# Optimization experiments

Measured on AMD Instinct MI355X. Metric: run time of the kernel, lower is better.

Reference implementation:

```python
import jax, jax.numpy as jnp
import numpy as np

N_NODES = 50000


def gcn_layer(x, W, b, src, dst, num_nodes):
    """PyG-style GCNConv: add self-loops, symmetric normalization, linear, scatter-add, bias."""
    # linear transform first (PyG applies lin before propagate)
    h = x @ W  # [N, out]
    # add self loops
    loop = jnp.arange(num_nodes, dtype=src.dtype)
    s = jnp.concatenate([src, loop])  # [E+N]
    d = jnp.concatenate([dst, loop])  # [E+N]
    # degree of target nodes (with self loops)
    deg = jax.ops.segment_sum(jnp.ones_like(d, dtype=h.dtype), d, num_segments=num_nodes)
    dis = jnp.where(deg > 0, jax.lax.rsqrt(deg), 0.0)  # deg^{-1/2}
    norm = dis[s] * dis[d]  # [E+N]
    msg = h[s] * norm[:, None]  # gather + scale: [E+N, out]
    out = jax.ops.segment_sum(msg, d, num_segments=num_nodes)  # scatter-add
    return out + b


def setup_inputs() -> dict:
    key = jax.random.key(0)
    ks = jax.random.split(key, 8)
    n, e = N_NODES, 800000
    in_c, hid_c, out_c = 64, 128, 64
    x = jax.random.normal(ks[0], (n, in_c), dtype=jnp.float32)
    edge_index = jax.random.randint(ks[1], (2, e), 0, n, dtype=jnp.int64)
    def glorot(k, fan_in, fan_out):
        lim = np.sqrt(6.0 / (fan_in + fan_out)).astype(np.float32)
        return jax.random.uniform(k, (fan_in, fan_out), jnp.float32, -lim, lim)
    return {
        "x": x,
        "edge_index": edge_index,
        "W1": glorot(ks[2], in_c, hid_c), "b1": jnp.zeros((hid_c,), jnp.float32),
        "W2": glorot(ks[3], hid_c, hid_c), "b2": jnp.zeros((hid_c,), jnp.float32),
        "W3": glorot(ks[4], hid_c, out_c), "b3": jnp.zeros((out_c,), jnp.float32),
    }


def reference(x, edge_index, W1, b1, W2, b2, W3, b3):
    src, dst = edge_index[0], edge_index[1]
    n = x.shape[0]
    h = gcn_layer(x, W1, b1, src, dst, n)
    h = jax.nn.relu(h)
    h = gcn_layer(h, W2, b2, src, dst, n)
    h = jax.nn.relu(h)
    return gcn_layer(h, W3, b3, src, dst, n)
```

## Files before the change

kernel.cpp:

```cpp
#include <hip/hip_runtime.h>
#include <hip/hip_fp16.h>


typedef _Float16 h8 __attribute__((ext_vector_type(8)));
typedef float f32x4 __attribute__((ext_vector_type(4)));

struct alignas(8) Half4 { __half2 lo, hi; };

__device__ inline float4 h4_to_f4(Half4 h) {
    float2 a = __half22float2(h.lo), b = __half22float2(h.hi);
    return make_float4(a.x, a.y, b.x, b.y);
}
__device__ inline Half4 f4_to_h4(float4 v) {
    Half4 h; h.lo = __floats2half2_rn(v.x, v.y); h.hi = __floats2half2_rn(v.z, v.w); return h;
}

#define MAXNB 512


__global__ __launch_bounds__(256) void bucket_count(const int* __restrict__ dst,
                                                    int* __restrict__ bcnt, int e, int nb) {
    __shared__ int h[MAXNB];
    int tid = threadIdx.x;
    for (int i = tid; i < nb; i += 256) h[i] = 0;
    __syncthreads();
    for (int i = blockIdx.x * 256 + tid; i < e; i += gridDim.x * 256)
        atomicAdd(&h[dst[i] >> 7], 1);
    __syncthreads();
    for (int i = tid; i < nb; i += 256) {
        int c = h[i];
        if (c) atomicAdd(&bcnt[i], c);
    }
}


__global__ void scan_buckets(const int* __restrict__ bcnt, int* __restrict__ bbase,
                             int* __restrict__ bcursor, int nb) {
    int lane = threadIdx.x;
    int running = 0;
    for (int base = 0; base < nb; base += 64) {
        int idx = base + lane;
        int v = (idx < nb) ? bcnt[idx] : 0;
        int x = v;
        #pragma unroll
        for (int d = 1; d < 64; d <<= 1) {
            int t = __shfl_up(x, d, 64);
            if (lane >= d) x += t;
        }
        if (idx < nb) { bbase[idx] = running + x - v; bcursor[idx] = running + x - v; }
        running += __shfl(x, 63, 64);
    }
    if (lane == 0) bbase[nb] = running;
}


#define R3_CHUNK 4096

template<bool PACKED>
__global__ __launch_bounds__(256) void bin_edges(const int* __restrict__ src,
                                                 const int* __restrict__ dst,
                                                 int* __restrict__ bcursor,
                                                 void* __restrict__ binned_, int e, int nb) {
    __shared__ int h[MAXNB];
    __shared__ int gp[MAXNB];
    int tid = threadIdx.x;
    for (int i = tid; i < nb; i += 256) h[i] = 0;
    __syncthreads();
    int lo = blockIdx.x * R3_CHUNK, hi = min(lo + R3_CHUNK, e);
    for (int i = lo + tid; i < hi; i += 256) atomicAdd(&h[dst[i] >> 7], 1);
    __syncthreads();
    for (int b = tid; b < nb; b += 256) {
        int c = h[b];
        if (c) gp[b] = atomicAdd(&bcursor[b], c);
        h[b] = 0;
    }
    __syncthreads();
    for (int i = lo + tid; i < hi; i += 256) {
        int d = dst[i];
        int b = d >> 7;
        int p = atomicAdd(&h[b], 1);
        if constexpr (PACKED)
            ((unsigned*)binned_)[gp[b] + p] = (unsigned)src[i] | ((unsigned)(d & 127) << 16);
        else
            ((int2*)binned_)[gp[b] + p] = make_int2(src[i], d);
    }
}


template<bool PACKED>
__global__ __launch_bounds__(128) void finalize_csr(const void* __restrict__ binned_,
                                                    const int* __restrict__ bbase,
                                                    int* __restrict__ offsets,
                                                    int* __restrict__ srcs,
                                                    float* __restrict__ dis,
                                                    const float* __restrict__ x,
                                                    Half4* __restrict__ x16,
                                                    int n, int nb) {
    int b = blockIdx.x;
    int tid = threadIdx.x;
    int nb0 = b << 7;
    int segLo = bbase[b], segHi = bbase[b + 1];

    __shared__ int cnt[128];
    __shared__ int cur[128];
    __shared__ float sdis[128];
    __shared__ int wtot;
    cnt[tid] = 0;
    __syncthreads();
    if constexpr (PACKED) {
        const unsigned* binned = (const unsigned*)binned_;
        for (int i = segLo + tid; i < segHi; i += 128)
            atomicAdd(&cnt[(binned[i] >> 16) & 127], 1);
    } else {
        const int2* binned = (const int2*)binned_;
        for (int i = segLo + tid; i < segHi; i += 128)
            atomicAdd(&cnt[binned[i].y & 127], 1);
    }
    __syncthreads();

    int c = cnt[tid];
    int lane = tid & 63, w = tid >> 6;
    int x_ = c;
    #pragma unroll
    for (int d = 1; d < 64; d <<= 1) {
        int t = __shfl_up(x_, d, 64);
        if (lane >= d) x_ += t;
    }
    if (w == 0 && lane == 63) wtot = x_;
    __syncthreads();
    int excl = x_ - c + (w ? wtot : 0);

    int node = nb0 + tid;
    float dv = rsqrtf((float)(c + 1));
    if (node < n) {
        offsets[node] = segLo + excl;
        dis[node] = dv;
    }
    if (b == nb - 1 && tid == 0) offsets[n] = segHi;
    cur[tid] = excl;
    sdis[tid] = dv;
    __syncthreads();

    if constexpr (PACKED) {
        const unsigned* binned = (const unsigned*)binned_;
        for (int i = segLo + tid; i < segHi; i += 128) {
            unsigned v = binned[i];
            int ln = (v >> 16) & 127;
            int p = atomicAdd(&cur[ln], 1);
            srcs[segLo + p] = (int)(v & 0xFFFFu);
        }
    } else {
        const int2* binned = (const int2*)binned_;
        for (int i = segLo + tid; i < segHi; i += 128) {
            int2 v = binned[i];
            int ln = v.y & 127;
            int p = atomicAdd(&cur[ln], 1);
            srcs[segLo + p] = v.x;
        }
    }

    int rows = min(128, n - nb0);
    if (rows > 0) {
        int limit = rows * 16;
        const float4* xr = reinterpret_cast<const float4*>(x) + (size_t)nb0 * 16;
        Half4* xo = x16 + (size_t)nb0 * 16;
        for (int idx = tid; idx < limit; idx += 128) {
            float d = sdis[idx >> 4];
            float4 v = xr[idx];
            xo[idx] = f4_to_h4(make_float4(v.x * d, v.y * d, v.z * d, v.w * d));
        }
    }
}


template<int C, bool RELU, bool BIAS, bool OUTH>
__global__ __launch_bounds__(256) void aggregate_h(const __half* __restrict__ g,
                                                   const int* __restrict__ srcs,
                                                   const int* __restrict__ offsets,
                                                   const float* __restrict__ dis,
                                                   const float* __restrict__ bias,
                                                   void* __restrict__ outv, int n) {
    int wid = threadIdx.x >> 6, lane = threadIdx.x & 63;
    int i = blockIdx.x * 4 + wid;
    if (i >= n) return;
    float di = dis[i];
    int e0 = offsets[i], e1 = offsets[i + 1];
    int e = e0;

    if constexpr (C == 128) {
        int half_ = lane >> 5, cl = lane & 31, c = cl * 4;
        const Half4* gc = reinterpret_cast<const Half4*>(g) + cl;
        float4 a0 = make_float4(0.f, 0.f, 0.f, 0.f), a1v = a0, a2 = a0, a3 = a0;

        if (half_ == 0) a0 = h4_to_f4(gc[(size_t)i * 32]);

        for (; e + 8 <= e1; e += 8) {
            int s0 = srcs[e + half_], s1 = srcs[e + 2 + half_];
            int s2 = srcs[e + 4 + half_], s3 = srcs[e + 6 + half_];
            float4 l0 = h4_to_f4(gc[(size_t)s0 * 32]);
            float4 l1 = h4_to_f4(gc[(size_t)s1 * 32]);
            float4 l2 = h4_to_f4(gc[(size_t)s2 * 32]);
            float4 l3 = h4_to_f4(gc[(size_t)s3 * 32]);
            a0.x += l0.x; a0.y += l0.y; a0.z += l0.z; a0.w += l0.w;
            a1v.x += l1.x; a1v.y += l1.y; a1v.z += l1.z; a1v.w += l1.w;
            a2.x += l2.x; a2.y += l2.y; a2.z += l2.z; a2.w += l2.w;
            a3.x += l3.x; a3.y += l3.y; a3.z += l3.z; a3.w += l3.w;
        }
        if (e + 4 <= e1) {
            int s0 = srcs[e + half_], s1 = srcs[e + 2 + half_];
            float4 l0 = h4_to_f4(gc[(size_t)s0 * 32]);
            float4 l1 = h4_to_f4(gc[(size_t)s1 * 32]);
            a0.x += l0.x; a0.y += l0.y; a0.z += l0.z; a0.w += l0.w;
            a1v.x += l1.x; a1v.y += l1.y; a1v.z += l1.z; a1v.w += l1.w;
            e += 4;
        }
        if (e + 2 <= e1) {
            int s0 = srcs[e + half_];
            float4 l0 = h4_to_f4(gc[(size_t)s0 * 32]);
            a2.x += l0.x; a2.y += l0.y; a2.z += l0.z; a2.w += l0.w;
            e += 2;
        }
        if (e < e1 && half_ == 0) {
            int s0 = srcs[e];
            float4 l0 = h4_to_f4(gc[(size_t)s0 * 32]);
            a3.x += l0.x; a3.y += l0.y; a3.z += l0.z; a3.w += l0.w;
        }

        float4 acc = make_float4((a0.x + a1v.x) + (a2.x + a3.x), (a0.y + a1v.y) + (a2.y + a3.y),
                                 (a0.z + a1v.z) + (a2.z + a3.z), (a0.w + a1v.w) + (a2.w + a3.w));
        acc.x += __shfl_xor(acc.x, 32, 64);
        acc.y += __shfl_xor(acc.y, 32, 64);
        acc.z += __shfl_xor(acc.z, 32, 64);
        acc.w += __shfl_xor(acc.w, 32, 64);

        if (half_ == 0) {
            float4 o = make_float4(di * acc.x, di * acc.y, di * acc.z, di * acc.w);
            if constexpr (BIAS) {
                float4 b = *reinterpret_cast<const float4*>(bias + c);
                o.x += b.x; o.y += b.y; o.z += b.z; o.w += b.w;
            }
            if constexpr (RELU) {
                o.x = fmaxf(o.x, 0.f); o.y = fmaxf(o.y, 0.f);
                o.z = fmaxf(o.z, 0.f); o.w = fmaxf(o.w, 0.f);
            }
            if constexpr (OUTH)
                *reinterpret_cast<Half4*>((__half*)outv + (size_t)i * C + c) = f4_to_h4(o);
            else
                *reinterpret_cast<float4*>((float*)outv + (size_t)i * C + c) = o;
        }
    } else {
        int grp = lane >> 4, cl = lane & 15, c = cl * 4;
        const Half4* gc = reinterpret_cast<const Half4*>(g) + cl;
        float4 a0 = make_float4(0.f, 0.f, 0.f, 0.f), a1v = a0;

        if (grp == 0) a0 = h4_to_f4(gc[(size_t)i * 16]);

        for (; e + 8 <= e1; e += 8) {
            int s0 = srcs[e + grp], s1 = srcs[e + 4 + grp];
            float4 l0 = h4_to_f4(gc[(size_t)s0 * 16]);
            float4 l1 = h4_to_f4(gc[(size_t)s1 * 16]);
            a0.x += l0.x; a0.y += l0.y; a0.z += l0.z; a0.w += l0.w;
            a1v.x += l1.x; a1v.y += l1.y; a1v.z += l1.z; a1v.w += l1.w;
        }
        if (e + 4 <= e1) {
            int s0 = srcs[e + grp];
            float4 l0 = h4_to_f4(gc[(size_t)s0 * 16]);
            a0.x += l0.x; a0.y += l0.y; a0.z += l0.z; a0.w += l0.w;
            e += 4;
        }
        int rem = e1 - e;
        if (grp < rem) {
            int s0 = srcs[e + grp];
            float4 l0 = h4_to_f4(gc[(size_t)s0 * 16]);
            a1v.x += l0.x; a1v.y += l0.y; a1v.z += l0.z; a1v.w += l0.w;
        }

        float4 acc = make_float4(a0.x + a1v.x, a0.y + a1v.y, a0.z + a1v.z, a0.w + a1v.w);
        #pragma unroll
        for (int d = 16; d <= 32; d <<= 1) {
            acc.x += __shfl_xor(acc.x, d, 64);
            acc.y += __shfl_xor(acc.y, d, 64);
            acc.z += __shfl_xor(acc.z, d, 64);
            acc.w += __shfl_xor(acc.w, d, 64);
        }

        if (grp == 0) {
            float4 o = make_float4(di * acc.x, di * acc.y, di * acc.z, di * acc.w);
            if constexpr (BIAS) {
                float4 b = *reinterpret_cast<const float4*>(bias + c);
                o.x += b.x; o.y += b.y; o.z += b.z; o.w += b.w;
            }
            if constexpr (RELU) {
                o.x = fmaxf(o.x, 0.f); o.y = fmaxf(o.y, 0.f);
                o.z = fmaxf(o.z, 0.f); o.w = fmaxf(o.w, 0.f);
            }
            if constexpr (OUTH)
                *reinterpret_cast<Half4*>((__half*)outv + (size_t)i * C + c) = f4_to_h4(o);
            else
                *reinterpret_cast<float4*>((float*)outv + (size_t)i * C + c) = o;
        }
    }
}


template<int CIN, int COUT>
__device__ inline void pack_frag(const float* __restrict__ W, h8* __restrict__ Wp, int idx) {
    constexpr int NCT = COUT / 16;
    int l = idx & 63;
    int ct = (idx >> 6) % NCT;
    int ks = (idx >> 6) / NCT;
    int col = ct * 16 + (l & 15);
    int kb = ks * 32 + ((l >> 4) << 2);
    h8 t;
    #pragma unroll
    for (int j = 0; j < 8; ++j) {
        int k = kb + (j & 3) + ((j >> 2) << 4);
        t[j] = (_Float16)W[k * COUT + col];
    }
    Wp[idx] = t;
}

__global__ __launch_bounds__(256) void pack_all(const float* __restrict__ W1,
                                                const float* __restrict__ W2,
                                                const float* __restrict__ W3,
                                                h8* __restrict__ Wp1, h8* __restrict__ Wp2,
                                                h8* __restrict__ Wp3, int* __restrict__ bcnt) {
    int idx = blockIdx.x * 256 + threadIdx.x;
    if (idx < 1024)      pack_frag<64, 128>(W1, Wp1, idx);
    else if (idx < 3072) pack_frag<128, 128>(W2, Wp2, idx - 1024);
    else if (idx < 4096) pack_frag<128, 64>(W3, Wp3, idx - 3072);
    else {
        int z = idx - 4096;
        if (z < MAXNB) { bcnt[z] = 0; if (z + 256 < MAXNB) bcnt[z + 256] = 0; }
    }
}


template<int CIN, int COUT, int EPI>
__global__ __launch_bounds__(256) void mfma_gemm(const __half* __restrict__ A,
                                                 const h8* __restrict__ Wp,
                                                 const float* __restrict__ aux,
                                                 __half* __restrict__ out, int n) {
    constexpr int NKS = CIN / 32, NCT = COUT / 16;
    constexpr int FRAGS = NKS * NCT * 64;
    __shared__ h8 wlds[FRAGS];
    for (int idx = threadIdx.x; idx < FRAGS; idx += 256) wlds[idx] = Wp[idx];
    __syncthreads();

    int wid = threadIdx.x >> 6, lane = threadIdx.x & 63;
    int rowBase = blockIdx.x * 128 + wid * 32;
    int m = lane & 15;
    int kq = (lane >> 4) << 2;

    int row0 = min(rowBase + m, n - 1);
    int row1 = min(rowBase + 16 + m, n - 1);
    const __half* ar0 = A + (size_t)row0 * CIN;
    const __half* ar1 = A + (size_t)row1 * CIN;

    f32x4 acc[2][NCT];
    #pragma unroll
    for (int rt = 0; rt < 2; ++rt)
        #pragma unroll
        for (int ct = 0; ct < NCT; ++ct)
            acc[rt][ct] = f32x4{0.f, 0.f, 0.f, 0.f};

    #pragma unroll
    for (int ks = 0; ks < NKS; ++ks) {
        int kb = ks * 32 + kq;
        h8 a0, a1;
        *reinterpret_cast<short4*>(&a0) = *reinterpret_cast<const short4*>(ar0 + kb);
        *(reinterpret_cast<short4*>(&a0) + 1) = *reinterpret_cast<const short4*>(ar0 + kb + 16);
        *reinterpret_cast<short4*>(&a1) = *reinterpret_cast<const short4*>(ar1 + kb);
        *(reinterpret_cast<short4*>(&a1) + 1) = *reinterpret_cast<const short4*>(ar1 + kb + 16);
        #pragma unroll
        for (int ct = 0; ct < NCT; ++ct) {
            h8 b = wlds[(ks * NCT + ct) * 64 + lane];
            acc[0][ct] = __builtin_amdgcn_mfma_f32_16x16x32_f16(a0, b, acc[0][ct], 0, 0, 0);
            acc[1][ct] = __builtin_amdgcn_mfma_f32_16x16x32_f16(a1, b, acc[1][ct], 0, 0, 0);
        }
    }

    float bcol[NCT];
    if constexpr (EPI == 1) {
        #pragma unroll
        for (int ct = 0; ct < NCT; ++ct) bcol[ct] = aux[ct * 16 + m];
    }
    #pragma unroll
    for (int rt = 0; rt < 2; ++rt) {
        #pragma unroll
        for (int r = 0; r < 4; ++r) {
            int row = rowBase + rt * 16 + kq + r;
            if (row < n) {
                float d = 0.f;
                if constexpr (EPI == 0) d = aux[row];
                __half* orow = out + (size_t)row * COUT + m;
                #pragma unroll
                for (int ct = 0; ct < NCT; ++ct) {
                    float v = acc[rt][ct][r];
                    if constexpr (EPI == 0) v *= d;
                    else v = fmaxf(v + bcol[ct], 0.f);
                    orow[ct * 16] = __float2half(v);
                }
            }
        }
    }
}


extern "C" void kernel_launch(void* const* d_in, const int* in_sizes, int n_in,
                              void* d_out, int out_size, void* d_ws, size_t ws_size,
                              hipStream_t stream) {
    const float* x  = (const float*)d_in[0];
    const int*   ei = (const int*)d_in[1];
    const float* W1 = (const float*)d_in[2];
    const float* b1 = (const float*)d_in[3];
    const float* W2 = (const float*)d_in[4];
    const float* b2 = (const float*)d_in[5];
    const float* W3 = (const float*)d_in[6];
    const float* b3 = (const float*)d_in[7];

    const int n = in_sizes[0] / 64;
    const int e = in_sizes[1] / 2;
    const int* src = ei;
    const int* dst = ei + e;
    const int nb = (n + 127) >> 7;
    const bool packed = (n <= 65536);

    int*   ws_i = (int*)d_ws;
    float* ws_f = (float*)d_ws;
    size_t o = 0;
    int* bcnt    = ws_i + o; o += MAXNB;
    int* bbase   = ws_i + o; o += MAXNB + 2;
    int* bcursor = ws_i + o; o += MAXNB;
    int* offsets = ws_i + o; o += n + 8;
    int* srcs    = ws_i + o; o += e;
    float* dis   = ws_f + o; o += n;
    o = (o + 1) & ~(size_t)1;
    void* binned = (void*)(ws_i + o); o += (size_t)e * 2;
    o = (o + 3) & ~(size_t)3;
    h8* Wp1 = (h8*)(ws_i + o); o += 4096;
    h8* Wp2 = (h8*)(ws_i + o); o += 8192;
    h8* Wp3 = (h8*)(ws_i + o); o += 4096;
    float* R1 = ws_f + o; o += (size_t)n * 64;
    float* R2 = ws_f + o; o += (size_t)n * 64;

    Half4*  x16 = (Half4*)d_out;
    __half* g2  = (__half*)d_out;
    __half* a1h = (__half*)R1;
    __half* h1h = (__half*)R2;
    __half* h2h = (__half*)R1;
    __half* g3  = (__half*)R2;
    float*  out = (float*)d_out;

    const int B = 256;
    pack_all<<<17, B, 0, stream>>>(W1, W2, W3, Wp1, Wp2, Wp3, bcnt);
    bucket_count<<<256, B, 0, stream>>>(dst, bcnt, e, nb);
    scan_buckets<<<1, 64, 0, stream>>>(bcnt, bbase, bcursor, nb);
    if (packed) {
        bin_edges<true><<<(e + R3_CHUNK - 1) / R3_CHUNK, B, 0, stream>>>(src, dst, bcursor, binned, e, nb);
        finalize_csr<true><<<nb, 128, 0, stream>>>(binned, bbase, offsets, srcs, dis, x, x16, n, nb);
    } else {
        bin_edges<false><<<(e + R3_CHUNK - 1) / R3_CHUNK, B, 0, stream>>>(src, dst, bcursor, binned, e, nb);
        finalize_csr<false><<<nb, 128, 0, stream>>>(binned, bbase, offsets, srcs, dis, x, x16, n, nb);
    }

    dim3 agrid((n + 3) / 4);
    dim3 ggrid((n + 127) / 128);

    aggregate_h<64, false, false, true><<<agrid, 256, 0, stream>>>((const __half*)x16, srcs, offsets, dis, nullptr, a1h, n);
    mfma_gemm<64, 128, 1><<<ggrid, 256, 0, stream>>>(a1h, Wp1, b1, h1h, n);
    mfma_gemm<128, 128, 0><<<ggrid, 256, 0, stream>>>(h1h, Wp2, dis, g2, n);
    aggregate_h<128, true, true, true><<<agrid, 256, 0, stream>>>(g2, srcs, offsets, dis, b2, h2h, n);
    mfma_gemm<128, 64, 0><<<ggrid, 256, 0, stream>>>(h2h, Wp3, dis, g3, n);
    aggregate_h<64, false, true, false><<<agrid, 256, 0, stream>>>(g3, srcs, offsets, dis, b3, out, n);
}
```

Before: 174.7 us.

## Use 16-bit CSR source indices and 16-byte half8 gathers in aggregation

Stores CSR source indices as unsigned short when the node count fits in 16 bits, halving index traffic in the three aggregation kernels. The aggregation kernel is also unified across channel widths to load 8 halves (16 bytes) per lane instead of 4, so fewer lanes cover each row and more edges are gathered in parallel per wavefront. The launch sequence is duplicated per index type. The wider per-lane accumulators raise register use, and the extra shuffle stages lengthen the reduction.

```diff
diff --git a/kernel.cpp b/kernel.cpp
--- a/kernel.cpp
+++ b/kernel.cpp
@@ -7,10 +7,6 @@
 
 struct alignas(8) Half4 { __half2 lo, hi; };
 
-__device__ inline float4 h4_to_f4(Half4 h) {
-    float2 a = __half22float2(h.lo), b = __half22float2(h.hi);
-    return make_float4(a.x, a.y, b.x, b.y);
-}
 __device__ inline Half4 f4_to_h4(float4 v) {
     Half4 h; h.lo = __floats2half2_rn(v.x, v.y); h.hi = __floats2half2_rn(v.z, v.w); return h;
 }
@@ -91,7 +87,7 @@
 __global__ __launch_bounds__(128) void finalize_csr(const void* __restrict__ binned_,
                                                     const int* __restrict__ bbase,
                                                     int* __restrict__ offsets,
-                                                    int* __restrict__ srcs,
+                                                    void* __restrict__ srcs_,
                                                     float* __restrict__ dis,
                                                     const float* __restrict__ x,
                                                     Half4* __restrict__ x16,
@@ -143,14 +139,16 @@
 
     if constexpr (PACKED) {
         const unsigned* binned = (const unsigned*)binned_;
+        unsigned short* srcs = (unsigned short*)srcs_;
         for (int i = segLo + tid; i < segHi; i += 128) {
             unsigned v = binned[i];
             int ln = (v >> 16) & 127;
             int p = atomicAdd(&cur[ln], 1);
-            srcs[segLo + p] = (int)(v & 0xFFFFu);
+            srcs[segLo + p] = (unsigned short)(v & 0xFFFFu);
         }
     } else {
         const int2* binned = (const int2*)binned_;
+        int* srcs = (int*)srcs_;
         for (int i = segLo + tid; i < segHi; i += 128) {
             int2 v = binned[i];
             int ln = v.y & 127;
@@ -173,13 +171,16 @@
 }
 
 
-template<int C, bool RELU, bool BIAS, bool OUTH>
+template<int C, bool RELU, bool BIAS, bool OUTH, typename IT>
 __global__ __launch_bounds__(256) void aggregate_h(const __half* __restrict__ g,
-                                                   const int* __restrict__ srcs,
+                                                   const IT* __restrict__ srcs,
                                                    const int* __restrict__ offsets,
                                                    const float* __restrict__ dis,
                                                    const float* __restrict__ bias,
                                                    void* __restrict__ outv, int n) {
+    constexpr int LPR = C / 8;
+    constexpr int NG = 64 / LPR;
+    constexpr int RSTRIDE = C / 8;
     int wid = threadIdx.x >> 6, lane = threadIdx.x & 63;
     int i = blockIdx.x * 4 + wid;
     if (i >= n) return;
@@ -187,117 +188,69 @@
     int e0 = offsets[i], e1 = offsets[i + 1];
     int e = e0;
 
-    if constexpr (C == 128) {
-        int half_ = lane >> 5, cl = lane & 31, c = cl * 4;
-        const Half4* gc = reinterpret_cast<const Half4*>(g) + cl;
-        float4 a0 = make_float4(0.f, 0.f, 0.f, 0.f), a1v = a0, a2 = a0, a3 = a0;
-
-        if (half_ == 0) a0 = h4_to_f4(gc[(size_t)i * 32]);
-
-        for (; e + 8 <= e1; e += 8) {
-            int s0 = srcs[e + half_], s1 = srcs[e + 2 + half_];
-            int s2 = srcs[e + 4 + half_], s3 = srcs[e + 6 + half_];
-            float4 l0 = h4_to_f4(gc[(size_t)s0 * 32]);
-            float4 l1 = h4_to_f4(gc[(size_t)s1 * 32]);
-            float4 l2 = h4_to_f4(gc[(size_t)s2 * 32]);
-            float4 l3 = h4_to_f4(gc[(size_t)s3 * 32]);
-            a0.x += l0.x; a0.y += l0.y; a0.z += l0.z; a0.w += l0.w;
-            a1v.x += l1.x; a1v.y += l1.y; a1v.z += l1.z; a1v.w += l1.w;
-            a2.x += l2.x; a2.y += l2.y; a2.z += l2.z; a2.w += l2.w;
-            a3.x += l3.x; a3.y += l3.y; a3.z += l3.z; a3.w += l3.w;
-        }
-        if (e + 4 <= e1) {
-            int s0 = srcs[e + half_], s1 = srcs[e + 2 + half_];
-            float4 l0 = h4_to_f4(gc[(size_t)s0 * 32]);
-            float4 l1 = h4_to_f4(gc[(size_t)s1 * 32]);
-            a0.x += l0.x; a0.y += l0.y; a0.z += l0.z; a0.w += l0.w;
-            a1v.x += l1.x; a1v.y += l1.y; a1v.z += l1.z; a1v.w += l1.w;
-            e += 4;
-        }
-        if (e + 2 <= e1) {
-            int s0 = srcs[e + half_];
-            float4 l0 = h4_to_f4(gc[(size_t)s0 * 32]);
-            a2.x += l0.x; a2.y += l0.y; a2.z += l0.z; a2.w += l0.w;
-            e += 2;
-        }
-        if (e < e1 && half_ == 0) {
-            int s0 = srcs[e];
-            float4 l0 = h4_to_f4(gc[(size_t)s0 * 32]);
-            a3.x += l0.x; a3.y += l0.y; a3.z += l0.z; a3.w += l0.w;
-        }
-
-        float4 acc = make_float4((a0.x + a1v.x) + (a2.x + a3.x), (a0.y + a1v.y) + (a2.y + a3.y),
-                                 (a0.z + a1v.z) + (a2.z + a3.z), (a0.w + a1v.w) + (a2.w + a3.w));
-        acc.x += __shfl_xor(acc.x, 32, 64);
-        acc.y += __shfl_xor(acc.y, 32, 64);
-        acc.z += __shfl_xor(acc.z, 32, 64);
-        acc.w += __shfl_xor(acc.w, 32, 64);
-
-        if (half_ == 0) {
-            float4 o = make_float4(di * acc.x, di * acc.y, di * acc.z, di * acc.w);
-            if constexpr (BIAS) {
-                float4 b = *reinterpret_cast<const float4*>(bias + c);
-                o.x += b.x; o.y += b.y; o.z += b.z; o.w += b.w;
-            }
-            if constexpr (RELU) {
-                o.x = fmaxf(o.x, 0.f); o.y = fmaxf(o.y, 0.f);
-                o.z = fmaxf(o.z, 0.f); o.w = fmaxf(o.w, 0.f);
-            }
-            if constexpr (OUTH)
-                *reinterpret_cast<Half4*>((__half*)outv + (size_t)i * C + c) = f4_to_h4(o);
-            else
-                *reinterpret_cast<float4*>((float*)outv + (size_t)i * C + c) = o;
-        }
-    } else {
-        int grp = lane >> 4, cl = lane & 15, c = cl * 4;
-        const Half4* gc = reinterpret_cast<const Half4*>(g) + cl;
-        float4 a0 = make_float4(0.f, 0.f, 0.f, 0.f), a1v = a0;
-
-        if (grp == 0) a0 = h4_to_f4(gc[(size_t)i * 16]);
-
-        for (; e + 8 <= e1; e += 8) {
-            int s0 = srcs[e + grp], s1 = srcs[e + 4 + grp];
-            float4 l0 = h4_to_f4(gc[(size_t)s0 * 16]);
-            float4 l1 = h4_to_f4(gc[(size_t)s1 * 16]);
-            a0.x += l0.x; a0.y += l0.y; a0.z += l0.z; a0.w += l0.w;
-            a1v.x += l1.x; a1v.y += l1.y; a1v.z += l1.z; a1v.w += l1.w;
-        }
-        if (e + 4 <= e1) {
-            int s0 = srcs[e + grp];
-            float4 l0 = h4_to_f4(gc[(size_t)s0 * 16]);
-            a0.x += l0.x; a0.y += l0.y; a0.z += l0.z; a0.w += l0.w;
-            e += 4;
-        }
-        int rem = e1 - e;
-        if (grp < rem) {
-            int s0 = srcs[e + grp];
-            float4 l0 = h4_to_f4(gc[(size_t)s0 * 16]);
-            a1v.x += l0.x; a1v.y += l0.y; a1v.z += l0.z; a1v.w += l0.w;
-        }
-
-        float4 acc = make_float4(a0.x + a1v.x, a0.y + a1v.y, a0.z + a1v.z, a0.w + a1v.w);
-        #pragma unroll
-        for (int d = 16; d <= 32; d <<= 1) {
-            acc.x += __shfl_xor(acc.x, d, 64);
-            acc.y += __shfl_xor(acc.y, d, 64);
-            acc.z += __shfl_xor(acc.z, d, 64);
-            acc.w += __shfl_xor(acc.w, d, 64);
-        }
-
-        if (grp == 0) {
-            float4 o = make_float4(di * acc.x, di * acc.y, di * acc.z, di * acc.w);
-            if constexpr (BIAS) {
-                float4 b = *reinterpret_cast<const float4*>(bias + c);
-                o.x += b.x; o.y += b.y; o.z += b.z; o.w += b.w;
-            }
-            if constexpr (RELU) {
-                o.x = fmaxf(o.x, 0.f); o.y = fmaxf(o.y, 0.f);
-                o.z = fmaxf(o.z, 0.f); o.w = fmaxf(o.w, 0.f);
-            }
-            if constexpr (OUTH)
-                *reinterpret_cast<Half4*>((__half*)outv + (size_t)i * C + c) = f4_to_h4(o);
-            else
-                *reinterpret_cast<float4*>((float*)outv + (size_t)i * C + c) = o;
+    int grp = lane / LPR, cl = lane % LPR;
+    const h8* gc = reinterpret_cast<const h8*>(g) + cl;
+
+    float a0[8], a1[8];
+    #pragma unroll
+    for (int j = 0; j < 8; ++j) { a0[j] = 0.f; a1[j] = 0.f; }
+
+    if (grp == 0) {
+        h8 v = gc[(size_t)i * RSTRIDE];
+        #pragma unroll
+        for (int j = 0; j < 8; ++j) a0[j] = (float)v[j];
+    }
+
+    for (; e + 2 * NG <= e1; e += 2 * NG) {
+        int s0 = (int)srcs[e + grp], s1 = (int)srcs[e + NG + grp];
+        h8 l0 = gc[(size_t)s0 * RSTRIDE];
+        h8 l1 = gc[(size_t)s1 * RSTRIDE];
+        #pragma unroll
+        for (int j = 0; j < 8; ++j) { a0[j] += (float)l0[j]; a1[j] += (float)l1[j]; }
+    }
+    if (e + NG <= e1) {
+        int s0 = (int)srcs[e + grp];
+        h8 l0 = gc[(size_t)s0 * RSTRIDE];
+        #pragma unroll
+        for (int j = 0; j < 8; ++j) a0[j] += (float)l0[j];
+        e += NG;
+    }
+    int rem = e1 - e;
+    if (grp < rem) {
+        int s0 = (int)srcs[e + grp];
+        h8 l0 = gc[(size_t)s0 * RSTRIDE];
+        #pragma unroll
+        for (int j = 0; j < 8; ++j) a1[j] += (float)l0[j];
+    }
+
+    float acc[8];
+    #pragma unroll
+    for (int j = 0; j < 8; ++j) acc[j] = a0[j] + a1[j];
+    #pragma unroll
+    for (int d = LPR; d < 64; d <<= 1) {
+        #pragma unroll
+        for (int j = 0; j < 8; ++j) acc[j] += __shfl_xor(acc[j], d, 64);
+    }
+
+    if (grp == 0) {
+        int c = cl * 8;
+        float o[8];
+        #pragma unroll
+        for (int j = 0; j < 8; ++j) {
+            float t = di * acc[j];
+            if constexpr (BIAS) t += bias[c + j];
+            if constexpr (RELU) t = fmaxf(t, 0.f);
+            o[j] = t;
+        }
+        if constexpr (OUTH) {
+            h8 hv;
+            #pragma unroll
+            for (int j = 0; j < 8; ++j) hv[j] = (_Float16)o[j];
+            reinterpret_cast<h8*>((__half*)outv)[(size_t)i * RSTRIDE + cl] = hv;
+        } else {
+            float* op = (float*)outv + (size_t)i * C + c;
+            *reinterpret_cast<float4*>(op) = make_float4(o[0], o[1], o[2], o[3]);
+            *reinterpret_cast<float4*>(op + 4) = make_float4(o[4], o[5], o[6], o[7]);
         }
     }
 }
@@ -433,7 +386,7 @@
     int* bbase   = ws_i + o; o += MAXNB + 2;
     int* bcursor = ws_i + o; o += MAXNB;
     int* offsets = ws_i + o; o += n + 8;
-    int* srcs    = ws_i + o; o += e;
+    void* srcs   = (void*)(ws_i + o); o += e;
     float* dis   = ws_f + o; o += n;
     o = (o + 1) & ~(size_t)1;
     void* binned = (void*)(ws_i + o); o += (size_t)e * 2;
@@ -456,21 +409,29 @@
     pack_all<<<17, B, 0, stream>>>(W1, W2, W3, Wp1, Wp2, Wp3, bcnt);
     bucket_count<<<256, B, 0, stream>>>(dst, bcnt, e, nb);
     scan_buckets<<<1, 64, 0, stream>>>(bcnt, bbase, bcursor, nb);
+
+    dim3 agrid((n + 3) / 4);
+    dim3 ggrid((n + 127) / 128);
+
     if (packed) {
         bin_edges<true><<<(e + R3_CHUNK - 1) / R3_CHUNK, B, 0, stream>>>(src, dst, bcursor, binned, e, nb);
         finalize_csr<true><<<nb, 128, 0, stream>>>(binned, bbase, offsets, srcs, dis, x, x16, n, nb);
+        const unsigned short* s16 = (const unsigned short*)srcs;
+        aggregate_h<64, false, false, true, unsigned short><<<agrid, 256, 0, stream>>>((const __half*)x16, s16, offsets, dis, nullptr, a1h, n);
+        mfma_gemm<64, 128, 1><<<ggrid, 256, 0, stream>>>(a1h, Wp1, b1, h1h, n);
+        mfma_gemm<128, 128, 0><<<ggrid, 256, 0, stream>>>(h1h, Wp2, dis, g2, n);
+        aggregate_h<128, true, true, true, unsigned short><<<agrid, 256, 0, stream>>>(g2, s16, offsets, dis, b2, h2h, n);
+        mfma_gemm<128, 64, 0><<<ggrid, 256, 0, stream>>>(h2h, Wp3, dis, g3, n);
+        aggregate_h<64, false, true, false, unsigned short><<<agrid, 256, 0, stream>>>(g3, s16, offsets, dis, b3, out, n);
     } else {
         bin_edges<false><<<(e + R3_CHUNK - 1) / R3_CHUNK, B, 0, stream>>>(src, dst, bcursor, binned, e, nb);
         finalize_csr<false><<<nb, 128, 0, stream>>>(binned, bbase, offsets, srcs, dis, x, x16, n, nb);
-    }
-
-    dim3 agrid((n + 3) / 4);
-    dim3 ggrid((n + 127) / 128);
-
-    aggregate_h<64, false, false, true><<<agrid, 256, 0, stream>>>((const __half*)x16, srcs, offsets, dis, nullptr, a1h, n);
-    mfma_gemm<64, 128, 1><<<ggrid, 256, 0, stream>>>(a1h, Wp1, b1, h1h, n);
-    mfma_gemm<128, 128, 0><<<ggrid, 256, 0, stream>>>(h1h, Wp2, dis, g2, n);
-    aggregate_h<128, true, true, true><<<agrid, 256, 0, stream>>>(g2, srcs, offsets, dis, b2, h2h, n);
-    mfma_gemm<128, 64, 0><<<ggrid, 256, 0, stream>>>(h2h, Wp3, dis, g3, n);
-    aggregate_h<64, false, true, false><<<agrid, 256, 0, stream>>>(g3, srcs, offsets, dis, b3, out, n);
-}
+        const int* s32 = (const int*)srcs;
+        aggregate_h<64, false, false, true, int><<<agrid, 256, 0, stream>>>((const __half*)x16, s32, offsets, dis, nullptr, a1h, n);
+        mfma_gemm<64, 128, 1><<<ggrid, 256, 0, stream>>>(a1h, Wp1, b1, h1h, n);
+        mfma_gemm<128, 128, 0><<<ggrid, 256, 0, stream>>>(h1h, Wp2, dis, g2, n);
+        aggregate_h<128, true, true, true, int><<<agrid, 256, 0, stream>>>(g2, s32, offsets, dis, b2, h2h, n);
+        mfma_gemm<128, 64, 0><<<ggrid, 256, 0, stream>>>(h2h, Wp3, dis, g3, n);
+        aggregate_h<64, false, true, false, int><<<agrid, 256, 0, stream>>>(g3, s32, offsets, dis, b3, out, n);
+    }
+}
```

Result: faster. 168.2 us (-3.7%).
